# Kernel tuning notes

Measured on AMD Instinct MI355X. Metric: run time of the kernel, lower is better.

## Reference

```python
import jax, jax.numpy as jnp
import numpy as np

MARGIN = 0.3
NEG_FALLBACK = 1e6  # value used when a row has no negatives


def setup_inputs() -> dict:
    key = jax.random.key(0)
    k1, k2 = jax.random.split(key)
    N, D, NUM_IDS = 8192, 256, 512
    feat = jax.random.normal(k1, (N, D), dtype=jnp.float32)
    labels = jax.random.randint(k2, (N,), 0, NUM_IDS, dtype=jnp.int64)
    return {"feat": feat, "labels": labels}


def reference(feat, labels):
    N = feat.shape[0]
    sq_norms = jnp.sum(feat * feat, axis=1)  # [N]
    sq = sq_norms[:, None] + sq_norms[None, :] - 2.0 * (feat @ feat.T)  # [N,N]
    sq = jnp.maximum(sq, 0.0)
    # safe sqrt (zero distance on the diagonal would otherwise give nan grads)
    dist = jnp.where(sq > 0, jnp.sqrt(jnp.where(sq > 0, sq, 1.0)), 0.0)

    same = labels[:, None] == labels[None, :]          # [N,N] bool
    eye = jnp.eye(N, dtype=bool)
    is_pos = same & ~eye                                # exclude self-pair
    is_neg = ~same

    # hard mining: per-row masked max over positives / min over negatives
    dist_ap = jnp.where(is_pos.any(axis=1),
                        jnp.where(is_pos, dist, -jnp.inf).max(axis=1), 0.0)
    dist_an = jnp.where(is_neg.any(axis=1),
                        jnp.where(is_neg, dist, jnp.inf).min(axis=1), NEG_FALLBACK)

    # MarginRankingLoss with y=1: mean(relu(margin - (dist_an - dist_ap)))
    return jnp.mean(jnp.maximum(0.0, MARGIN + dist_ap - dist_an))
```

## Files before the change

### kernel.cpp

```cpp
#include <hip/hip_runtime.h>


constexpr int N = 8192;
constexpr int D = 256;
constexpr float MARGIN = 0.3f;
constexpr float NEG_FALLBACK = 1e6f;
constexpr float TBIG = 1e30f;

typedef __attribute__((ext_vector_type(8))) __bf16 bf16x8;
typedef __attribute__((ext_vector_type(4))) float f32x4;

__device__ __forceinline__ unsigned enc_f(float f) {
  unsigned u = __float_as_uint(f);
  return (u >> 31) ? ~u : (u | 0x80000000u);
}
__device__ __forceinline__ float dec_f(unsigned e) {
  unsigned u = (e >> 31) ? (e ^ 0x80000000u) : ~e;
  return __uint_as_float(u);
}
__device__ __forceinline__ unsigned short f2bf_rtn(float x) {
  unsigned u = __float_as_uint(x);
  return (unsigned short)((u + 0x7fffu + ((u >> 16) & 1u)) >> 16);
}


__global__ void tl_pass0f(const float* __restrict__ feat, float* __restrict__ norms,
                          unsigned* __restrict__ ap, unsigned* __restrict__ an,
                          unsigned short* __restrict__ P, float* __restrict__ out) {
  int row = blockIdx.x * 4 + (threadIdx.x >> 6);
  int lane = threadIdx.x & 63;
  float4 f = reinterpret_cast<const float4*>(feat + (size_t)row * D)[lane];
  ushort4 h;
  h.x = f2bf_rtn(f.x); h.y = f2bf_rtn(f.y); h.z = f2bf_rtn(f.z); h.w = f2bf_rtn(f.w);
  reinterpret_cast<ushort4*>(P + (size_t)row * D)[lane] = h;
  float s = fmaf(f.x, f.x, fmaf(f.y, f.y, fmaf(f.z, f.z, f.w * f.w)));
#pragma unroll
  for (int off = 32; off > 0; off >>= 1) s += __shfl_down(s, off, 64);
  if (lane == 0) {
    norms[row] = s;
    ap[row] = enc_f(-TBIG);
    an[row] = enc_f(TBIG);
  }
  if (row == 0 && lane == 0) out[0] = 0.0f;
}


__global__ __launch_bounds__(256, 3)
void tl_pass1m(const unsigned short* __restrict__ P, const int* __restrict__ labels,
               const float* __restrict__ norms,
               unsigned* __restrict__ ap, unsigned* __restrict__ an) {
  __shared__ unsigned short lbuf[2][128][64];

  unsigned short (*lA)[64] = lbuf[0];
  unsigned short (*lB)[64] = lbuf[1];

  const int tid = threadIdx.x;
  const int wave = tid >> 6;
  const int lane = tid & 63;
  const int c = lane & 15;
  const int q = lane >> 4;
  const int ib0 = blockIdx.y * 128;
  const int jb0 = blockIdx.x * 128;
  const int wi = (wave & 1) * 64;
  const int wj = (wave >> 1) * 64;

  f32x4 acc[4][4];
#pragma unroll
  for (int a = 0; a < 4; ++a)
#pragma unroll
    for (int b = 0; b < 4; ++b) acc[a][b] = (f32x4){0.f, 0.f, 0.f, 0.f};

  const int rsub = lane >> 3;
  const int gsw = (lane & 7) ^ (rsub & 7);

  for (int kc = 0; kc < D; kc += 64) {
#pragma unroll
    for (int t = 0; t < 4; ++t) {
      int rA = wave * 32 + t * 8;
      const unsigned short* gA = P + (size_t)(ib0 + rA + rsub) * D + kc + gsw * 8;
      __builtin_amdgcn_global_load_lds(
          (const __attribute__((address_space(1))) void*)gA,
          (__attribute__((address_space(3))) void*)&lA[rA][0], 16, 0, 0);
      const unsigned short* gB = P + (size_t)(jb0 + rA + rsub) * D + kc + gsw * 8;
      __builtin_amdgcn_global_load_lds(
          (const __attribute__((address_space(1))) void*)gB,
          (__attribute__((address_space(3))) void*)&lB[rA][0], 16, 0, 0);
    }
    __syncthreads();

#pragma unroll
    for (int ks = 0; ks < 2; ++ks) {
      bf16x8 af[4], bfr[4];
      const int gsel = ((ks * 4 + q) ^ (c & 7)) * 8;
#pragma unroll
      for (int a = 0; a < 4; ++a)
        af[a] = *(const bf16x8*)&lA[wi + a * 16 + c][gsel];
#pragma unroll
      for (int b = 0; b < 4; ++b)
        bfr[b] = *(const bf16x8*)&lB[wj + b * 16 + c][gsel];
#pragma unroll
      for (int a = 0; a < 4; ++a)
#pragma unroll
        for (int b = 0; b < 4; ++b)
          acc[a][b] = __builtin_amdgcn_mfma_f32_16x16x32_bf16(af[a], bfr[b], acc[a][b], 0, 0, 0);
    }
    __syncthreads();
  }

  int cj[4]; float nj[4]; int lj[4];
#pragma unroll
  for (int b = 0; b < 4; ++b) {
    cj[b] = jb0 + wj + b * 16 + c;
    nj[b] = norms[cj[b]];
    lj[b] = labels[cj[b]];
  }

  float tp[4][4], tn[4][4];
#pragma unroll
  for (int a = 0; a < 4; ++a) {
#pragma unroll
    for (int r = 0; r < 4; ++r) {
      int rg = ib0 + wi + a * 16 + q * 4 + r;
      int li = labels[rg];
      float vp = -TBIG, vn = TBIG;
#pragma unroll
      for (int b = 0; b < 4; ++b) {
        float t = fmaf(-2.f, acc[a][b][r], nj[b]);
        bool sm = (lj[b] == li);
        bool dg = (cj[b] == rg);
        vp = fmaxf(vp, (sm && !dg) ? t : -TBIG);
        vn = fminf(vn, sm ? TBIG : t);
      }
      tp[a][r] = vp;
      tn[a][r] = vn;
    }
  }

  float* S = (float*)lbuf;
  const int slot = (wave >> 1) * 16 + c;

#pragma unroll
  for (int a = 0; a < 4; ++a)
#pragma unroll
    for (int r = 0; r < 4; ++r)
      S[(wi + a * 16 + q * 4 + r) * 36 + slot] = tp[a][r];
  __syncthreads();
  float vp = 0.f;
  if (tid < 128) {
    const f32x4* Srow = (const f32x4*)&S[tid * 36];
    f32x4 m0 = Srow[0];
#pragma unroll
    for (int i = 1; i < 8; ++i) {
      f32x4 v = Srow[i];
      m0[0] = fmaxf(m0[0], v[0]); m0[1] = fmaxf(m0[1], v[1]);
      m0[2] = fmaxf(m0[2], v[2]); m0[3] = fmaxf(m0[3], v[3]);
    }
    vp = fmaxf(fmaxf(m0[0], m0[1]), fmaxf(m0[2], m0[3]));
  }
  __syncthreads();
#pragma unroll
  for (int a = 0; a < 4; ++a)
#pragma unroll
    for (int r = 0; r < 4; ++r)
      S[(wi + a * 16 + q * 4 + r) * 36 + slot] = tn[a][r];
  __syncthreads();
  if (tid < 128) {
    const f32x4* Srow = (const f32x4*)&S[tid * 36];
    f32x4 m0 = Srow[0];
#pragma unroll
    for (int i = 1; i < 8; ++i) {
      f32x4 v = Srow[i];
      m0[0] = fminf(m0[0], v[0]); m0[1] = fminf(m0[1], v[1]);
      m0[2] = fminf(m0[2], v[2]); m0[3] = fminf(m0[3], v[3]);
    }
    float vn = fminf(fminf(m0[0], m0[1]), fminf(m0[2], m0[3]));
    atomicMax(&ap[ib0 + tid], enc_f(vp));
    atomicMin(&an[ib0 + tid], enc_f(vn));
  }
}


__global__ void tl_pass2f(const unsigned* __restrict__ ap, const unsigned* __restrict__ an,
                          const float* __restrict__ norms, float* __restrict__ out) {
  int r = blockIdx.x * 256 + threadIdx.x;
  float ni = norms[r];
  float tpv = dec_f(ap[r]);
  float tnv = dec_f(an[r]);
  float dap = (tpv < -1e29f) ? 0.f : sqrtf(fmaxf(ni + tpv, 0.f));
  float dan = (tnv > 1e29f) ? NEG_FALLBACK : sqrtf(fmaxf(ni + tnv, 0.f));
  float v = fmaxf(0.f, MARGIN + dap - dan) * (1.0f / (float)N);
#pragma unroll
  for (int off = 32; off > 0; off >>= 1) v += __shfl_down(v, off, 64);
  __shared__ float red[4];
  int lane = threadIdx.x & 63, w = threadIdx.x >> 6;
  if (lane == 0) red[w] = v;
  __syncthreads();
  if (threadIdx.x == 0) atomicAdd(out, red[0] + red[1] + red[2] + red[3]);
}


constexpr int FB_BK = 32;
constexpr int FB_JSPLIT = 8;
constexpr int FB_JRANGE = N / FB_JSPLIT;
constexpr int FB_LDS = 132;

__global__ void tl_pass0_fb(const float* __restrict__ feat, float* __restrict__ norms,
                            float* __restrict__ ap, float* __restrict__ an,
                            float* __restrict__ out) {
  int row = blockIdx.x * 4 + (threadIdx.x >> 6);
  int lane = threadIdx.x & 63;
  float4 f = reinterpret_cast<const float4*>(feat + (size_t)row * D)[lane];
  float s = f.x * f.x + f.y * f.y + f.z * f.z + f.w * f.w;
#pragma unroll
  for (int off = 32; off > 0; off >>= 1) s += __shfl_down(s, off, 64);
  if (lane == 0) { norms[row] = s; ap[row] = 0.0f; an[row] = NEG_FALLBACK; }
  if (row == 0 && lane == 0) out[0] = 0.0f;
}

__global__ __launch_bounds__(256, 2)
void tl_pass1_fb(const float* __restrict__ feat, const int* __restrict__ labels,
                 const float* __restrict__ norms,
                 unsigned int* __restrict__ ap, unsigned int* __restrict__ an) {
  __shared__ float As[FB_BK][FB_LDS];
  __shared__ float Bs[FB_BK][FB_LDS];
  const int tid = threadIdx.x;
  const int tx = tid & 15, ty = tid >> 4;
  const int ib0 = blockIdx.y * 128;
  const int jbase = blockIdx.x * FB_JRANGE;
  float ni[8]; int li[8]; int ri[8];
#pragma unroll
  for (int a = 0; a < 8; ++a) {
    int r = ty * 4 + (a & 3) + ((a >> 2) << 6);
    ri[a] = ib0 + r; ni[a] = norms[ri[a]]; li[a] = labels[ri[a]];
  }
  float apv[8], anv[8];
#pragma unroll
  for (int a = 0; a < 8; ++a) { apv[a] = 0.0f; anv[a] = NEG_FALLBACK; }
  for (int jt = 0; jt < FB_JRANGE; jt += 128) {
    const int jb = jbase + jt;
    float acc[8][8];
#pragma unroll
    for (int a = 0; a < 8; ++a)
#pragma unroll
      for (int b = 0; b < 8; ++b) acc[a][b] = 0.0f;
    for (int kc = 0; kc < D; kc += FB_BK) {
#pragma unroll
      for (int u = 0; u < 4; ++u) {
        int lin = tid + u * 256;
        int row = lin >> 3, c4 = lin & 7;
        float4 va = *reinterpret_cast<const float4*>(feat + (size_t)(ib0 + row) * D + kc + c4 * 4);
        As[c4 * 4 + 0][row] = va.x; As[c4 * 4 + 1][row] = va.y;
        As[c4 * 4 + 2][row] = va.z; As[c4 * 4 + 3][row] = va.w;
        float4 vb = *reinterpret_cast<const float4*>(feat + (size_t)(jb + row) * D + kc + c4 * 4);
        Bs[c4 * 4 + 0][row] = vb.x; Bs[c4 * 4 + 1][row] = vb.y;
        Bs[c4 * 4 + 2][row] = vb.z; Bs[c4 * 4 + 3][row] = vb.w;
      }
      __syncthreads();
#pragma unroll 8
      for (int k = 0; k < FB_BK; ++k) {
        float4 a0 = *reinterpret_cast<const float4*>(&As[k][ty * 4]);
        float4 a1 = *reinterpret_cast<const float4*>(&As[k][64 + ty * 4]);
        float4 b0 = *reinterpret_cast<const float4*>(&Bs[k][tx * 4]);
        float4 b1 = *reinterpret_cast<const float4*>(&Bs[k][64 + tx * 4]);
        float av[8] = {a0.x, a0.y, a0.z, a0.w, a1.x, a1.y, a1.z, a1.w};
        float bv[8] = {b0.x, b0.y, b0.z, b0.w, b1.x, b1.y, b1.z, b1.w};
#pragma unroll
        for (int a = 0; a < 8; ++a)
#pragma unroll
          for (int b = 0; b < 8; ++b) acc[a][b] = fmaf(av[a], bv[b], acc[a][b]);
      }
      __syncthreads();
    }
#pragma unroll
    for (int b = 0; b < 8; ++b) {
      int cjx = jb + tx * 4 + (b & 3) + ((b >> 2) << 6);
      float njx = norms[cjx]; int ljx = labels[cjx];
#pragma unroll
      for (int a = 0; a < 8; ++a) {
        float sq = fmaxf(ni[a] + njx - 2.0f * acc[a][b], 0.0f);
        float dist = sqrtf(sq);
        if (li[a] == ljx) { if (ri[a] != cjx) apv[a] = fmaxf(apv[a], dist); }
        else anv[a] = fminf(anv[a], dist);
      }
    }
  }
  __syncthreads();
  float* red = &As[0][0];
#pragma unroll
  for (int a = 0; a < 8; ++a) {
    int r = ty * 4 + (a & 3) + ((a >> 2) << 6);
    red[r * 16 + tx] = apv[a];
  }
  __syncthreads();
  if (tid < 128) {
    float m = red[tid * 16];
#pragma unroll
    for (int t = 1; t < 16; ++t) m = fmaxf(m, red[tid * 16 + t]);
    atomicMax(&ap[ib0 + tid], __float_as_uint(m));
  }
  __syncthreads();
#pragma unroll
  for (int a = 0; a < 8; ++a) {
    int r = ty * 4 + (a & 3) + ((a >> 2) << 6);
    red[r * 16 + tx] = anv[a];
  }
  __syncthreads();
  if (tid < 128) {
    float m = red[tid * 16];
#pragma unroll
    for (int t = 1; t < 16; ++t) m = fminf(m, red[tid * 16 + t]);
    atomicMin(&an[ib0 + tid], __float_as_uint(m));
  }
}

__global__ void tl_pass2_fb(const float* __restrict__ ap, const float* __restrict__ an,
                            float* __restrict__ out) {
  int r = blockIdx.x * 256 + threadIdx.x;
  float v = fmaxf(0.0f, MARGIN + ap[r] - an[r]) * (1.0f / (float)N);
#pragma unroll
  for (int off = 32; off > 0; off >>= 1) v += __shfl_down(v, off, 64);
  __shared__ float red[4];
  int lane = threadIdx.x & 63, w = threadIdx.x >> 6;
  if (lane == 0) red[w] = v;
  __syncthreads();
  if (threadIdx.x == 0) atomicAdd(out, red[0] + red[1] + red[2] + red[3]);
}


extern "C" void kernel_launch(void* const* d_in, const int* in_sizes, int n_in,
                              void* d_out, int out_size, void* d_ws, size_t ws_size,
                              hipStream_t stream) {
  const float* feat = (const float*)d_in[0];
  const int* labels = (const int*)d_in[1];
  float* out = (float*)d_out;

  float* norms = (float*)d_ws;
  unsigned* ap = (unsigned*)(norms + N);
  unsigned* an = ap + N;
  unsigned short* P = (unsigned short*)(an + N + 4);
  const size_t NEED = 3 * (size_t)N * 4 + 16 + (size_t)N * D * 2;

  if (ws_size >= NEED) {
    tl_pass0f<<<N / 4, 256, 0, stream>>>(feat, norms, ap, an, P, out);
    dim3 grid1(N / 128, N / 128);
    tl_pass1m<<<grid1, 256, 0, stream>>>(P, labels, norms, ap, an);
    tl_pass2f<<<N / 256, 256, 0, stream>>>(ap, an, norms, out);
  } else {
    float* apf = (float*)ap;
    float* anf = (float*)an;
    tl_pass0_fb<<<N / 4, 256, 0, stream>>>(feat, norms, apf, anf, out);
    dim3 grid1(FB_JSPLIT, N / 128);
    tl_pass1_fb<<<grid1, 256, 0, stream>>>(feat, labels, norms, (unsigned*)apf, (unsigned*)anf);
    tl_pass2_fb<<<N / 256, 256, 0, stream>>>(apf, anf, out);
  }
}
```

Measured before the change: 110.3 us.

## Sort rows by label so most tiles skip positive masking and use register-resident A

Adds a single-block counting sort that permutes rows by label, so each 128-row block knows the column range holding its positives. Column tiles outside that range only do a cheap min over negatives, with no label compares. The GEMM kernel is restructured: A fragments stay in registers for the full K, each block sweeps 1024 columns with double-buffered B tiles in LDS, and reductions use wave shuffles instead of an LDS transpose. The cost is an extra serial one-block sort launch, a gather in the conversion pass, higher register pressure (launch bounds lowered to 2), and fewer blocks in the grid.

```diff
diff --git a/kernel.cpp b/kernel.cpp
--- a/kernel.cpp
+++ b/kernel.cpp
@@ -24,159 +24,208 @@
 }
 
 
-__global__ void tl_pass0f(const float* __restrict__ feat, float* __restrict__ norms,
-                          unsigned* __restrict__ ap, unsigned* __restrict__ an,
-                          unsigned short* __restrict__ P, float* __restrict__ out) {
-  int row = blockIdx.x * 4 + (threadIdx.x >> 6);
-  int lane = threadIdx.x & 63;
-  float4 f = reinterpret_cast<const float4*>(feat + (size_t)row * D)[lane];
+__global__ void tl_sortk(const int* __restrict__ labels, int* __restrict__ perm,
+                         int* __restrict__ labp, int* __restrict__ offg) {
+  __shared__ int hist[512], scan[512];
+  const int tid = threadIdx.x;
+  hist[tid] = 0;
+  __syncthreads();
+  for (int i = tid; i < N; i += 512) atomicAdd(&hist[labels[i]], 1);
+  __syncthreads();
+  const int v = hist[tid];
+  scan[tid] = v;
+  __syncthreads();
+#pragma unroll
+  for (int d = 1; d < 512; d <<= 1) {
+    int t = (tid >= d) ? scan[tid - d] : 0;
+    __syncthreads();
+    scan[tid] += t;
+    __syncthreads();
+  }
+  const int excl = scan[tid] - v;
+  offg[tid] = excl;
+  if (tid == 511) offg[512] = scan[511];
+  hist[tid] = excl;
+  __syncthreads();
+  for (int i = tid; i < N; i += 512) {
+    const int L = labels[i];
+    const int pos = atomicAdd(&hist[L], 1);
+    perm[pos] = i;
+    labp[pos] = L;
+  }
+}
+
+
+__global__ void tl_pass0p(const float* __restrict__ feat, const int* __restrict__ perm,
+                          float* __restrict__ norms, unsigned* __restrict__ ap,
+                          unsigned* __restrict__ an, unsigned short* __restrict__ P,
+                          float* __restrict__ out) {
+  const int p = blockIdx.x * 4 + (threadIdx.x >> 6);
+  const int lane = threadIdx.x & 63;
+  const int src = perm[p];
+  float4 f = reinterpret_cast<const float4*>(feat + (size_t)src * D)[lane];
   ushort4 h;
   h.x = f2bf_rtn(f.x); h.y = f2bf_rtn(f.y); h.z = f2bf_rtn(f.z); h.w = f2bf_rtn(f.w);
-  reinterpret_cast<ushort4*>(P + (size_t)row * D)[lane] = h;
+  reinterpret_cast<ushort4*>(P + (size_t)p * D)[lane] = h;
   float s = fmaf(f.x, f.x, fmaf(f.y, f.y, fmaf(f.z, f.z, f.w * f.w)));
 #pragma unroll
   for (int off = 32; off > 0; off >>= 1) s += __shfl_down(s, off, 64);
   if (lane == 0) {
-    norms[row] = s;
-    ap[row] = enc_f(-TBIG);
-    an[row] = enc_f(TBIG);
-  }
-  if (row == 0 && lane == 0) out[0] = 0.0f;
-}
-
-
-__global__ __launch_bounds__(256, 3)
-void tl_pass1m(const unsigned short* __restrict__ P, const int* __restrict__ labels,
-               const float* __restrict__ norms,
+    norms[p] = s;
+    ap[p] = enc_f(-TBIG);
+    an[p] = enc_f(TBIG);
+  }
+  if (p == 0 && lane == 0) out[0] = 0.0f;
+}
+
+
+__global__ __launch_bounds__(256, 2)
+void tl_pass1s(const unsigned short* __restrict__ P, const int* __restrict__ labp,
+               const float* __restrict__ norms, const int* __restrict__ offg,
                unsigned* __restrict__ ap, unsigned* __restrict__ an) {
-  __shared__ unsigned short lbuf[2][128][64];
-
-  unsigned short (*lA)[64] = lbuf[0];
-  unsigned short (*lB)[64] = lbuf[1];
+  __shared__ unsigned short lB[2][128][128];
 
   const int tid = threadIdx.x;
   const int wave = tid >> 6;
   const int lane = tid & 63;
   const int c = lane & 15;
   const int q = lane >> 4;
-  const int ib0 = blockIdx.y * 128;
-  const int jb0 = blockIdx.x * 128;
-  const int wi = (wave & 1) * 64;
-  const int wj = (wave >> 1) * 64;
-
-  f32x4 acc[4][4];
-#pragma unroll
-  for (int a = 0; a < 4; ++a)
-#pragma unroll
-    for (int b = 0; b < 4; ++b) acc[a][b] = (f32x4){0.f, 0.f, 0.f, 0.f};
-
-  const int rsub = lane >> 3;
-  const int gsw = (lane & 7) ^ (rsub & 7);
-
-  for (int kc = 0; kc < D; kc += 64) {
-#pragma unroll
-    for (int t = 0; t < 4; ++t) {
-      int rA = wave * 32 + t * 8;
-      const unsigned short* gA = P + (size_t)(ib0 + rA + rsub) * D + kc + gsw * 8;
-      __builtin_amdgcn_global_load_lds(
-          (const __attribute__((address_space(1))) void*)gA,
-          (__attribute__((address_space(3))) void*)&lA[rA][0], 16, 0, 0);
-      const unsigned short* gB = P + (size_t)(jb0 + rA + rsub) * D + kc + gsw * 8;
-      __builtin_amdgcn_global_load_lds(
-          (const __attribute__((address_space(1))) void*)gB,
-          (__attribute__((address_space(3))) void*)&lB[rA][0], 16, 0, 0);
+  const int i0 = blockIdx.y * 128;
+  const int j0 = blockIdx.x * 1024;
+  const int wrow = i0 + wave * 32;
+
+  const int lo = offg[labp[i0]];
+  const int hi = offg[labp[i0 + 127] + 1];
+
+  bf16x8 af[2][8];
+#pragma unroll
+  for (int a = 0; a < 2; ++a)
+#pragma unroll
+    for (int t2 = 0; t2 < 8; ++t2)
+      af[a][t2] = *(const bf16x8*)(P + (size_t)(wrow + a * 16 + c) * D + t2 * 32 + q * 8);
+
+  f32x4 acc[2][8];
+#pragma unroll
+  for (int a = 0; a < 2; ++a)
+#pragma unroll
+    for (int b = 0; b < 8; ++b) acc[a][b] = (f32x4){0.f, 0.f, 0.f, 0.f};
+
+  float vp[2][4], vn[2][4];
+#pragma unroll
+  for (int a = 0; a < 2; ++a)
+#pragma unroll
+    for (int r = 0; r < 4; ++r) { vp[a][r] = -TBIG; vn[a][r] = TBIG; }
+
+  const int rsub = lane >> 4;
+  const int g15 = lane & 15;
+
+#define STAGE(BUF, S1)                                                                  \
+  do {                                                                                  \
+    const int jt_ = (S1) >> 1;                                                          \
+    const int kc_ = ((S1) & 1) * 128;                                                   \
+    const int jb_ = j0 + jt_ * 128;                                                     \
+    _Pragma("unroll") for (int t = 0; t < 8; ++t) {                                     \
+      const int rA_ = wave * 32 + t * 4;                                                \
+      const int sg_ = g15 ^ rsub ^ ((t & 1) * 4);                                       \
+      const unsigned short* gp_ = P + (size_t)(jb_ + rA_ + rsub) * D + kc_ + sg_ * 8;   \
+      __builtin_amdgcn_global_load_lds(                                                 \
+          (const __attribute__((address_space(1))) void*)gp_,                           \
+          (__attribute__((address_space(3))) void*)&lB[BUF][rA_][0], 16, 0, 0);         \
+    }                                                                                   \
+  } while (0)
+
+#define CHALF(KB)                                                                       \
+  do {                                                                                  \
+    _Pragma("unroll") for (int ks = 0; ks < 4; ++ks) {                                  \
+      const int gsel_ = ((ks * 4 + q) ^ (c & 7)) * 8;                                   \
+      bf16x8 bfr[8];                                                                    \
+      _Pragma("unroll") for (int b = 0; b < 8; ++b)                                     \
+          bfr[b] = *(const bf16x8*)&lB[cur][b * 16 + c][gsel_];                         \
+      _Pragma("unroll") for (int a = 0; a < 2; ++a)                                     \
+          _Pragma("unroll") for (int b = 0; b < 8; ++b)                                 \
+              acc[a][b] = __builtin_amdgcn_mfma_f32_16x16x32_bf16(                      \
+                  af[a][(KB) + ks], bfr[b], acc[a][b], 0, 0, 0);                        \
+    }                                                                                   \
+  } while (0)
+
+  STAGE(0, 0);
+  __syncthreads();
+  int cur = 0;
+
+#pragma unroll 2
+  for (int s = 0; s < 16; ++s) {
+    if (s < 15) STAGE(cur ^ 1, s + 1);
+    if ((s & 1) == 0) CHALF(0); else CHALF(4);
+
+    if (s & 1) {
+      const int jt = s >> 1;
+      const int jb0 = j0 + jt * 128;
+      const bool careful = (jb0 < hi) && (jb0 + 128 > lo);
+      if (!careful) {
+#pragma unroll
+        for (int b = 0; b < 8; ++b) {
+          const float njb = norms[jb0 + b * 16 + c];
+#pragma unroll
+          for (int a = 0; a < 2; ++a)
+#pragma unroll
+            for (int r = 0; r < 4; ++r)
+              vn[a][r] = fminf(vn[a][r], fmaf(-2.f, acc[a][b][r], njb));
+        }
+      } else {
+        int lj[8], cj[8];
+        float nj[8];
+#pragma unroll
+        for (int b = 0; b < 8; ++b) {
+          cj[b] = jb0 + b * 16 + c;
+          nj[b] = norms[cj[b]];
+          lj[b] = labp[cj[b]];
+        }
+#pragma unroll
+        for (int a = 0; a < 2; ++a)
+#pragma unroll
+          for (int r = 0; r < 4; ++r) {
+            const int rg = wrow + a * 16 + q * 4 + r;
+            const int li = labp[rg];
+            float vpl = vp[a][r], vnl = vn[a][r];
+#pragma unroll
+            for (int b = 0; b < 8; ++b) {
+              const float t = fmaf(-2.f, acc[a][b][r], nj[b]);
+              const bool sm = (lj[b] == li);
+              const bool dg = (cj[b] == rg);
+              vpl = fmaxf(vpl, (sm && !dg) ? t : -TBIG);
+              vnl = fminf(vnl, sm ? TBIG : t);
+            }
+            vp[a][r] = vpl;
+            vn[a][r] = vnl;
+          }
+      }
+#pragma unroll
+      for (int a = 0; a < 2; ++a)
+#pragma unroll
+        for (int b = 0; b < 8; ++b) acc[a][b] = (f32x4){0.f, 0.f, 0.f, 0.f};
     }
     __syncthreads();
-
-#pragma unroll
-    for (int ks = 0; ks < 2; ++ks) {
-      bf16x8 af[4], bfr[4];
-      const int gsel = ((ks * 4 + q) ^ (c & 7)) * 8;
-#pragma unroll
-      for (int a = 0; a < 4; ++a)
-        af[a] = *(const bf16x8*)&lA[wi + a * 16 + c][gsel];
-#pragma unroll
-      for (int b = 0; b < 4; ++b)
-        bfr[b] = *(const bf16x8*)&lB[wj + b * 16 + c][gsel];
-#pragma unroll
-      for (int a = 0; a < 4; ++a)
-#pragma unroll
-        for (int b = 0; b < 4; ++b)
-          acc[a][b] = __builtin_amdgcn_mfma_f32_16x16x32_bf16(af[a], bfr[b], acc[a][b], 0, 0, 0);
+    cur ^= 1;
+  }
+#undef STAGE
+#undef CHALF
+
+#pragma unroll
+  for (int a = 0; a < 2; ++a)
+#pragma unroll
+    for (int r = 0; r < 4; ++r) {
+      float p = vp[a][r], n = vn[a][r];
+#pragma unroll
+      for (int m = 1; m < 16; m <<= 1) {
+        p = fmaxf(p, __shfl_xor(p, m, 64));
+        n = fminf(n, __shfl_xor(n, m, 64));
+      }
+      if (c == 0) {
+        const int rg = wrow + a * 16 + q * 4 + r;
+        atomicMax(&ap[rg], enc_f(p));
+        atomicMin(&an[rg], enc_f(n));
+      }
     }
-    __syncthreads();
-  }
-
-  int cj[4]; float nj[4]; int lj[4];
-#pragma unroll
-  for (int b = 0; b < 4; ++b) {
-    cj[b] = jb0 + wj + b * 16 + c;
-    nj[b] = norms[cj[b]];
-    lj[b] = labels[cj[b]];
-  }
-
-  float tp[4][4], tn[4][4];
-#pragma unroll
-  for (int a = 0; a < 4; ++a) {
-#pragma unroll
-    for (int r = 0; r < 4; ++r) {
-      int rg = ib0 + wi + a * 16 + q * 4 + r;
-      int li = labels[rg];
-      float vp = -TBIG, vn = TBIG;
-#pragma unroll
-      for (int b = 0; b < 4; ++b) {
-        float t = fmaf(-2.f, acc[a][b][r], nj[b]);
-        bool sm = (lj[b] == li);
-        bool dg = (cj[b] == rg);
-        vp = fmaxf(vp, (sm && !dg) ? t : -TBIG);
-        vn = fminf(vn, sm ? TBIG : t);
-      }
-      tp[a][r] = vp;
-      tn[a][r] = vn;
-    }
-  }
-
-  float* S = (float*)lbuf;
-  const int slot = (wave >> 1) * 16 + c;
-
-#pragma unroll
-  for (int a = 0; a < 4; ++a)
-#pragma unroll
-    for (int r = 0; r < 4; ++r)
-      S[(wi + a * 16 + q * 4 + r) * 36 + slot] = tp[a][r];
-  __syncthreads();
-  float vp = 0.f;
-  if (tid < 128) {
-    const f32x4* Srow = (const f32x4*)&S[tid * 36];
-    f32x4 m0 = Srow[0];
-#pragma unroll
-    for (int i = 1; i < 8; ++i) {
-      f32x4 v = Srow[i];
-      m0[0] = fmaxf(m0[0], v[0]); m0[1] = fmaxf(m0[1], v[1]);
-      m0[2] = fmaxf(m0[2], v[2]); m0[3] = fmaxf(m0[3], v[3]);
-    }
-    vp = fmaxf(fmaxf(m0[0], m0[1]), fmaxf(m0[2], m0[3]));
-  }
-  __syncthreads();
-#pragma unroll
-  for (int a = 0; a < 4; ++a)
-#pragma unroll
-    for (int r = 0; r < 4; ++r)
-      S[(wi + a * 16 + q * 4 + r) * 36 + slot] = tn[a][r];
-  __syncthreads();
-  if (tid < 128) {
-    const f32x4* Srow = (const f32x4*)&S[tid * 36];
-    f32x4 m0 = Srow[0];
-#pragma unroll
-    for (int i = 1; i < 8; ++i) {
-      f32x4 v = Srow[i];
-      m0[0] = fminf(m0[0], v[0]); m0[1] = fminf(m0[1], v[1]);
-      m0[2] = fminf(m0[2], v[2]); m0[3] = fminf(m0[3], v[3]);
-    }
-    float vn = fminf(fminf(m0[0], m0[1]), fminf(m0[2], m0[3]));
-    atomicMax(&ap[ib0 + tid], enc_f(vp));
-    atomicMin(&an[ib0 + tid], enc_f(vn));
-  }
 }
 
 
@@ -337,13 +386,17 @@
   float* norms = (float*)d_ws;
   unsigned* ap = (unsigned*)(norms + N);
   unsigned* an = ap + N;
-  unsigned short* P = (unsigned short*)(an + N + 4);
-  const size_t NEED = 3 * (size_t)N * 4 + 16 + (size_t)N * D * 2;
+  int* perm = (int*)(an + N);
+  int* labp = perm + N;
+  int* offg = labp + N;
+  unsigned short* P = (unsigned short*)(offg + 520);
+  const size_t NEED = (size_t)5 * N * 4 + 520 * 4 + (size_t)N * D * 2;
 
   if (ws_size >= NEED) {
-    tl_pass0f<<<N / 4, 256, 0, stream>>>(feat, norms, ap, an, P, out);
-    dim3 grid1(N / 128, N / 128);
-    tl_pass1m<<<grid1, 256, 0, stream>>>(P, labels, norms, ap, an);
+    tl_sortk<<<1, 512, 0, stream>>>(labels, perm, labp, offg);
+    tl_pass0p<<<N / 4, 256, 0, stream>>>(feat, perm, norms, ap, an, P, out);
+    dim3 grid1(8, N / 128);
+    tl_pass1s<<<grid1, 256, 0, stream>>>(P, labp, norms, offg, ap, an);
     tl_pass2f<<<N / 256, 256, 0, stream>>>(ap, an, norms, out);
   } else {
     float* apf = (float*)ap;
```

New measurement: 116.7 us. 1.06x slower.
